# Kernel optimization log

Hardware: AMD Instinct MI355X
Metric: run time of the kernel (lower is better)

## Reference

```python
import jax, jax.numpy as jnp
import numpy as np

B = 1024          # batch
C_LEAF = 2048     # leaf classes (prob vector length)
C_INT = 256       # internal-node classes
C_ALL = C_LEAF + C_INT
E = 12            # max edges on a root-to-leaf path (tree depth)


def setup_inputs() -> dict:
    key = jax.random.key(0)
    k1, k2, k3, k4, k5 = jax.random.split(key, 5)
    # class probabilities (flat softmax-like vector over leaves)
    x = jax.random.uniform(k1, (B, C_LEAF), dtype=jnp.float32) + 1e-3
    inputs = x / jnp.sum(x, axis=1, keepdims=True)
    target = jax.random.randint(k2, (B,), 0, C_ALL)
    # synthetic tree buffers: onehot_den is an elementwise superset of
    # onehot_num (true for the real tree: denominator subtree contains the
    # numerator subtree), so den >= num > 0 wherever num != 0.
    onehot_num = (jax.random.uniform(k3, (C_ALL, C_LEAF, E)) < 0.05).astype(jnp.float32)
    extra = (jax.random.uniform(k4, (C_ALL, C_LEAF, E)) < 0.10).astype(jnp.float32)
    onehot_den = jnp.clip(onehot_num + extra, 0.0, 1.0)
    weights = jax.random.uniform(k5, (C_ALL, E), dtype=jnp.float32)
    return {"inputs": inputs, "target": target,
            "onehot_num": onehot_num, "onehot_den": onehot_den,
            "weights": weights}


def reference(inputs, target, onehot_num, onehot_den, weights):
    # gather per-sample one-hot masks by target, then bmm: [b,1,c] @ [b,c,e] -> [b,e]
    num = jnp.einsum('bc,bce->be', inputs, onehot_num[target])
    den = jnp.einsum('bc,bce->be', inputs, onehot_den[target])
    safe = num != 0
    # num[idx] = -log(num/den) where num != 0, else keep 0
    val = jnp.where(safe,
                    -jnp.log(jnp.where(safe, num, 1.0) / jnp.where(safe, den, 1.0)),
                    0.0)
    # flip does not change the sum; kept for faithfulness to the original
    per_sample = jnp.sum(jnp.flip(weights[target] * val, axis=1), axis=1)
    return jnp.mean(per_sample)
```

## Files before the change

kernel.cpp:

```cpp
#include <hip/hip_runtime.h>

#define C_LEAF 2048
#define E_DIM  12
#define BLOCK  256

__global__ __launch_bounds__(BLOCK) void hll_fused(
    const float* __restrict__ inputs,
    const int*   __restrict__ target,
    const float* __restrict__ onum,
    const float* __restrict__ oden,
    const float* __restrict__ weights,
    float*       __restrict__ out,
    int B)
{
    const int b = blockIdx.x;
    const int t = target[b];

    const float* __restrict__ xrow = inputs + (size_t)b * C_LEAF;
    const float* __restrict__ nrow = onum + (size_t)t * C_LEAF * E_DIM;
    const float* __restrict__ drow = oden + (size_t)t * C_LEAF * E_DIM;

    float accn[E_DIM], accd[E_DIM];
#pragma unroll
    for (int e = 0; e < E_DIM; ++e) { accn[e] = 0.f; accd[e] = 0.f; }

    for (int c = threadIdx.x; c < C_LEAF; c += BLOCK) {
        const float x = xrow[c];
        const float4* __restrict__ n4 = (const float4*)(nrow + (size_t)c * E_DIM);
        const float4* __restrict__ d4 = (const float4*)(drow + (size_t)c * E_DIM);
#pragma unroll
        for (int q = 0; q < 3; ++q) {
            const float4 nv = n4[q];
            const float4 dv = d4[q];
            accn[4*q+0] += x * nv.x; accn[4*q+1] += x * nv.y;
            accn[4*q+2] += x * nv.z; accn[4*q+3] += x * nv.w;
            accd[4*q+0] += x * dv.x; accd[4*q+1] += x * dv.y;
            accd[4*q+2] += x * dv.z; accd[4*q+3] += x * dv.w;
        }
    }

#pragma unroll
    for (int e = 0; e < E_DIM; ++e) {
#pragma unroll
        for (int off = 32; off >= 1; off >>= 1) {
            accn[e] += __shfl_xor(accn[e], off, 64);
            accd[e] += __shfl_xor(accd[e], off, 64);
        }
    }

    __shared__ float sn[4][E_DIM];
    __shared__ float sd[4][E_DIM];
    const int wave = threadIdx.x >> 6;
    const int lane = threadIdx.x & 63;
    if (lane == 0) {
#pragma unroll
        for (int e = 0; e < E_DIM; ++e) { sn[wave][e] = accn[e]; sd[wave][e] = accd[e]; }
    }
    __syncthreads();

    if (threadIdx.x == 0) {
        const float* __restrict__ w = weights + (size_t)t * E_DIM;
        float s = 0.f;
#pragma unroll
        for (int e = 0; e < E_DIM; ++e) {
            const float n = sn[0][e] + sn[1][e] + sn[2][e] + sn[3][e];
            const float d = sd[0][e] + sd[1][e] + sd[2][e] + sd[3][e];
            if (n != 0.f) s += w[e] * (-__logf(n / d));
        }
        atomicAdd(out, s / (float)B);
    }
}

extern "C" void kernel_launch(void* const* d_in, const int* in_sizes, int n_in,
                              void* d_out, int out_size, void* d_ws, size_t ws_size,
                              hipStream_t stream) {
    const float* inputs  = (const float*)d_in[0];
    const int*   target  = (const int*)  d_in[1];
    const float* onum    = (const float*)d_in[2];
    const float* oden    = (const float*)d_in[3];
    const float* weights = (const float*)d_in[4];
    float* out = (float*)d_out;

    const int B = in_sizes[1];

    (void)hipMemsetAsync(out, 0, sizeof(float), stream);
    hll_fused<<<B, BLOCK, 0, stream>>>(inputs, target, onum, oden, weights, out, B);
}
```

Baseline: 46.10 us.

## Replace atomic mean with per-sample buffer plus reduce kernel; unroll leaf loop by two

```diff
diff --git a/kernel.cpp b/kernel.cpp
--- a/kernel.cpp
+++ b/kernel.cpp
@@ -4,15 +4,14 @@
 #define E_DIM  12
 #define BLOCK  256
 
-__global__ __launch_bounds__(BLOCK) void hll_fused(
+__global__ __launch_bounds__(BLOCK) void hll_per_sample(
     const float* __restrict__ inputs,
     const int*   __restrict__ target,
     const float* __restrict__ onum,
     const float* __restrict__ oden,
     const float* __restrict__ weights,
-    float*       __restrict__ out,
-    int B)
-{
+    float*       __restrict__ per_sample
+) {
     const int b = blockIdx.x;
     const int t = target[b];
 
@@ -24,18 +23,30 @@
 #pragma unroll
     for (int e = 0; e < E_DIM; ++e) { accn[e] = 0.f; accd[e] = 0.f; }
 
-    for (int c = threadIdx.x; c < C_LEAF; c += BLOCK) {
-        const float x = xrow[c];
-        const float4* __restrict__ n4 = (const float4*)(nrow + (size_t)c * E_DIM);
-        const float4* __restrict__ d4 = (const float4*)(drow + (size_t)c * E_DIM);
+#pragma unroll
+    for (int it = 0; it < C_LEAF / BLOCK; it += 2) {
+        const int c0 = it * BLOCK + threadIdx.x;
+        const int c1 = c0 + BLOCK;
+        const float x0 = xrow[c0];
+        const float x1 = xrow[c1];
+        const float4* __restrict__ n40 = (const float4*)(nrow + (size_t)c0 * E_DIM);
+        const float4* __restrict__ d40 = (const float4*)(drow + (size_t)c0 * E_DIM);
+        const float4* __restrict__ n41 = (const float4*)(nrow + (size_t)c1 * E_DIM);
+        const float4* __restrict__ d41 = (const float4*)(drow + (size_t)c1 * E_DIM);
 #pragma unroll
         for (int q = 0; q < 3; ++q) {
-            const float4 nv = n4[q];
-            const float4 dv = d4[q];
-            accn[4*q+0] += x * nv.x; accn[4*q+1] += x * nv.y;
-            accn[4*q+2] += x * nv.z; accn[4*q+3] += x * nv.w;
-            accd[4*q+0] += x * dv.x; accd[4*q+1] += x * dv.y;
-            accd[4*q+2] += x * dv.z; accd[4*q+3] += x * dv.w;
+            const float4 nv0 = n40[q];
+            const float4 dv0 = d40[q];
+            const float4 nv1 = n41[q];
+            const float4 dv1 = d41[q];
+            accn[4*q+0] += x0 * nv0.x; accn[4*q+1] += x0 * nv0.y;
+            accn[4*q+2] += x0 * nv0.z; accn[4*q+3] += x0 * nv0.w;
+            accd[4*q+0] += x0 * dv0.x; accd[4*q+1] += x0 * dv0.y;
+            accd[4*q+2] += x0 * dv0.z; accd[4*q+3] += x0 * dv0.w;
+            accn[4*q+0] += x1 * nv1.x; accn[4*q+1] += x1 * nv1.y;
+            accn[4*q+2] += x1 * nv1.z; accn[4*q+3] += x1 * nv1.w;
+            accd[4*q+0] += x1 * dv1.x; accd[4*q+1] += x1 * dv1.y;
+            accd[4*q+2] += x1 * dv1.z; accd[4*q+3] += x1 * dv1.w;
         }
     }
 
@@ -67,8 +78,23 @@
             const float d = sd[0][e] + sd[1][e] + sd[2][e] + sd[3][e];
             if (n != 0.f) s += w[e] * (-__logf(n / d));
         }
-        atomicAdd(out, s / (float)B);
+        per_sample[b] = s;
     }
+}
+
+__global__ __launch_bounds__(64) void hll_reduce_mean(
+    const float* __restrict__ per_sample, float* __restrict__ out, int n)
+{
+    const float4* __restrict__ p4 = (const float4*)per_sample;
+    const int n4 = n >> 2;
+    float acc = 0.f;
+    for (int i = threadIdx.x; i < n4; i += 64) {
+        const float4 v = p4[i];
+        acc += (v.x + v.y) + (v.z + v.w);
+    }
+#pragma unroll
+    for (int off = 32; off >= 1; off >>= 1) acc += __shfl_xor(acc, off, 64);
+    if (threadIdx.x == 0) out[0] = acc / (float)n;
 }
 
 extern "C" void kernel_launch(void* const* d_in, const int* in_sizes, int n_in,
@@ -82,7 +108,8 @@
     float* out = (float*)d_out;
 
     const int B = in_sizes[1];
+    float* per_sample = (float*)d_ws;
 
-    (void)hipMemsetAsync(out, 0, sizeof(float), stream);
-    hll_fused<<<B, BLOCK, 0, stream>>>(inputs, target, onum, oden, weights, out, B);
+    hll_per_sample<<<B, BLOCK, 0, stream>>>(inputs, target, onum, oden, weights, per_sample);
+    hll_reduce_mean<<<1, 64, 0, stream>>>(per_sample, out, B);
 }
```

After: 46.39 us. About the same (+0.6%).
